# Kernel optimization log

Hardware: AMD Instinct MI355X
Metric: run time of the kernel (lower is better)

The kernel has to match this reference:

```python
import jax, jax.numpy as jnp
import numpy as np

B, C, H, W = 8, 256, 128, 128
SH, SW = 8, 8            # stoken_size
HH, WW = H // SH, W // SW
NH = 8                   # num_heads
HD = C // NH             # head_dim = 32
KD = HD                  # key_dim (attn_ratio=1)
ATTN_SCALE = KD ** (-0.5)
AFF_SCALE = C ** (-0.5)


def unfold9(x):
    """x: (B,C,hh,ww) -> (B, hh*ww, C, 9); matches Unfold(3) + transpose/reshape."""
    b, c, hh, ww = x.shape
    xp = jnp.pad(x, ((0, 0), (0, 0), (1, 1), (1, 1)))
    p = jnp.stack([xp[:, :, dy:dy + hh, dx:dx + ww]
                   for dy in range(3) for dx in range(3)], axis=2)  # (B,C,9,hh,ww)
    return p.transpose(0, 3, 4, 1, 2).reshape(b, hh * ww, c, 9)


def fold9(y):
    """y: (B,C,9,hh,ww) -> (B,C,hh,ww); matches Fold(3) (conv_transpose with identity kernels)."""
    hh, ww = y.shape[-2:]
    yp = jnp.pad(y, ((0, 0), (0, 0), (0, 0), (1, 1), (1, 1)))
    out = 0.
    for dy in range(3):
        for dx in range(3):
            out = out + yp[:, :, dy * 3 + dx, 2 - dy:2 - dy + hh, 2 - dx:2 - dx + ww]
    return out


def attention(sf, w_qkv, w_pe, w_proj):
    """Attention module with attn_ratio=1 (Conv layers have act=False, BN identity)."""
    b, c, hh, ww = sf.shape
    n = hh * ww
    qkv = jnp.einsum('oc,bchw->bohw', w_qkv, sf).reshape(b, NH, 2 * KD + HD, n)
    q, k, v = jnp.split(qkv, [KD, 2 * KD], axis=2)
    attn = jax.nn.softmax(jnp.einsum('bhkn,bhkm->bhnm', q, k) * ATTN_SCALE, axis=-1)
    o = jnp.einsum('bhdm,bhnm->bhdn', v, attn).reshape(b, c, hh, ww)
    pe = jax.lax.conv_general_dilated(
        v.reshape(b, c, hh, ww), w_pe, (1, 1), ((1, 1), (1, 1)),
        dimension_numbers=('NCHW', 'OIHW', 'NCHW'), feature_group_count=c)
    return jnp.einsum('oc,bchw->bohw', w_proj, o + pe)


def setup_inputs() -> dict:
    key = jax.random.key(0)
    k0, k1, k2, k3 = jax.random.split(key, 4)
    x = jax.random.normal(k0, (B, C, H, W), dtype=jnp.float32)
    w_qkv = jax.random.normal(k1, (3 * C, C), dtype=jnp.float32) * 0.05
    w_pe = jax.random.normal(k2, (C, 1, 3, 3), dtype=jnp.float32) * 0.05
    w_proj = jax.random.normal(k3, (C, C), dtype=jnp.float32) * 0.05
    return {'x': x, 'w_qkv': w_qkv, 'w_pe': w_pe, 'w_proj': w_proj}


def reference(x, w_qkv, w_pe, w_proj):
    # H,W divisible by stoken_size -> no padding branch
    xb = x.reshape(B, C, HH, SH, WW, SW)
    stoken = xb.mean(axis=(3, 5))                                   # (B,C,hh,ww) adaptive_avg_pool2d
    pix = xb.transpose(0, 2, 4, 3, 5, 1).reshape(B, HH * WW, SH * SW, C)
    # --- single no-grad iteration (n_iter=1) ---
    sf9 = unfold9(stoken)                                            # (B,n,C,9)
    aff = jax.nn.softmax(jnp.einsum('bnpc,bnck->bnpk', pix, sf9) * AFF_SCALE, axis=-1)
    aff = jax.lax.stop_gradient(aff)                                 # torch.no_grad
    asum = aff.sum(axis=2).transpose(0, 2, 1).reshape(B, 1, 9, HH, WW)
    asum = jax.lax.stop_gradient(fold9(asum))                        # (B,1,hh,ww)
    # --- super-token aggregation ---
    sf = jnp.einsum('bnpc,bnpk->bnck', pix, aff)                     # (B,n,C,9)
    sf = fold9(sf.transpose(0, 2, 3, 1).reshape(B, C, 9, HH, WW))    # (B,C,hh,ww)
    sf = sf / (asum + 1e-12)
    # --- refine with attention ---
    sf = attention(sf, w_qkv, w_pe, w_proj)
    # --- scatter back to pixels ---
    sf9b = unfold9(sf)                                               # (B,n,C,9)
    pix_out = jnp.einsum('bnck,bnpk->bnpc', sf9b, aff)               # (B,n,h*w,C)
    return pix_out.reshape(B, HH, WW, C, SH, SW).transpose(0, 3, 1, 4, 2, 5).reshape(B, C, H, W)
```

## Files before the change

kernel.cpp:

```cpp
#include <hip/hip_runtime.h>
#include <cstdint>
#include <cstddef>


#define AFF_SCALE 0.0625f
#define ATTN_SCALE 0.17677669529663687f

__global__ __launch_bounds__(128) void stoken_kernel(
    const float* __restrict__ x, float* __restrict__ stok_pad)
{
    int blk = blockIdx.x;
    int i  = blk & 15;
    int bc = blk >> 4;
    int t  = threadIdx.x;
    const float* xr = x + ((size_t)bc * 128 + i * 8) * 128 + t;
    float s = 0.f;
#pragma unroll
    for (int r = 0; r < 8; ++r) s += xr[r * 128];
    s += __shfl_down(s, 4, 64);
    s += __shfl_down(s, 2, 64);
    s += __shfl_down(s, 1, 64);
    if ((t & 7) == 0) {
        int j = t >> 3;
        stok_pad[((size_t)bc * 18 + (i + 1)) * 18 + (j + 1)] = s * (1.f / 64.f);
    }
}

__global__ __launch_bounds__(256) void aff_agg_kernel(
    const float* __restrict__ x, const float* __restrict__ stok_pad,
    float* __restrict__ aff_g, float* __restrict__ asum_g,
    float* __restrict__ agg)
{
    __shared__ float pixs[256 * 65];
    __shared__ float part[4 * 64 * 9];
    __shared__ float affs[9 * 64];

    int bn = blockIdx.x;
    int n = bn & 255, b = bn >> 8;
    int i = n >> 4, j = n & 15;
    int t = threadIdx.x;

    {
        int c0 = t >> 3, pi = t & 7;
#pragma unroll
        for (int it = 0; it < 8; ++it) {
            int c = c0 + 32 * it;
            const float* xp = x + (((size_t)b * 256 + c) * 128 + i * 8 + pi) * 128 + j * 8;
            const float4 f0 = *(const float4*)&xp[0];
            const float4 f1 = *(const float4*)&xp[4];
            float* d = &pixs[c * 65 + pi * 8];
            d[0] = f0.x; d[1] = f0.y; d[2] = f0.z; d[3] = f0.w;
            d[4] = f1.x; d[5] = f1.y; d[6] = f1.z; d[7] = f1.w;
        }
    }
    __syncthreads();

    int s = t >> 6, p = t & 63;
    float acc[9] = {0.f,0.f,0.f,0.f,0.f,0.f,0.f,0.f,0.f};
    {
        const float* sp = stok_pad + ((size_t)b * 256 + s * 64) * 324 + i * 18 + j;
        for (int cc = 0; cc < 64; ++cc) {
            float px = pixs[(s * 64 + cc) * 65 + p];
            const float* q = sp + cc * 324;
            acc[0] += px * q[0];  acc[1] += px * q[1];  acc[2] += px * q[2];
            acc[3] += px * q[18]; acc[4] += px * q[19]; acc[5] += px * q[20];
            acc[6] += px * q[36]; acc[7] += px * q[37]; acc[8] += px * q[38];
        }
    }
#pragma unroll
    for (int k = 0; k < 9; ++k) part[(s * 64 + p) * 9 + k] = acc[k];
    __syncthreads();

    if (t < 64) {
        float a[9];
        float mx = -1e30f;
#pragma unroll
        for (int k = 0; k < 9; ++k) {
            float v = (part[(0 * 64 + t) * 9 + k] + part[(1 * 64 + t) * 9 + k] +
                       part[(2 * 64 + t) * 9 + k] + part[(3 * 64 + t) * 9 + k]) * AFF_SCALE;
            a[k] = v;
            mx = fmaxf(mx, v);
        }
        float ssum = 0.f;
#pragma unroll
        for (int k = 0; k < 9; ++k) { a[k] = __expf(a[k] - mx); ssum += a[k]; }
        float inv = 1.f / ssum;
#pragma unroll
        for (int k = 0; k < 9; ++k) {
            a[k] *= inv;
            affs[k * 64 + t] = a[k];
            aff_g[(size_t)bn * 576 + k * 64 + t] = a[k];
        }
#pragma unroll
        for (int k = 0; k < 9; ++k) {
            float r = a[k];
            r += __shfl_down(r, 32, 64); r += __shfl_down(r, 16, 64);
            r += __shfl_down(r, 8, 64);  r += __shfl_down(r, 4, 64);
            r += __shfl_down(r, 2, 64);  r += __shfl_down(r, 1, 64);
            if (t == 0) asum_g[(size_t)bn * 9 + k] = r;
        }
    }
    __syncthreads();

    {
        int c = t;
        float a9[9] = {0.f,0.f,0.f,0.f,0.f,0.f,0.f,0.f,0.f};
        for (int p4 = 0; p4 < 16; ++p4) {
            float px0 = pixs[c * 65 + p4 * 4 + 0];
            float px1 = pixs[c * 65 + p4 * 4 + 1];
            float px2 = pixs[c * 65 + p4 * 4 + 2];
            float px3 = pixs[c * 65 + p4 * 4 + 3];
#pragma unroll
            for (int k = 0; k < 9; ++k) {
                const float4 av = *(const float4*)&affs[k * 64 + p4 * 4];
                a9[k] += px0 * av.x + px1 * av.y + px2 * av.z + px3 * av.w;
            }
        }
#pragma unroll
        for (int k = 0; k < 9; ++k)
            agg[((size_t)bn * 9 + k) * 256 + c] = a9[k];
    }
}

__global__ __launch_bounds__(256) void fold_div_kernel(
    const float* __restrict__ agg, const float* __restrict__ asum_g,
    float* __restrict__ sf)
{
    __shared__ float v[256 * 17];
    int b = blockIdx.x >> 4, y = blockIdx.x & 15;
    int t = threadIdx.x;
    for (int x = 0; x < 16; ++x) {
        float af = 0.f, val = 0.f;
#pragma unroll
        for (int dy = 0; dy < 3; ++dy)
#pragma unroll
            for (int dx = 0; dx < 3; ++dx) {
                int ii = y + 1 - dy, jj = x + 1 - dx;
                if ((unsigned)ii < 16u && (unsigned)jj < 16u) {
                    int idx = (b * 256 + ii * 16 + jj) * 9 + dy * 3 + dx;
                    af  += asum_g[idx];
                    val += agg[(size_t)idx * 256 + t];
                }
            }
        v[t * 17 + x] = val / (af + 1e-12f);
    }
    __syncthreads();
    int xw = t & 15, cw0 = t >> 4;
#pragma unroll
    for (int it = 0; it < 16; ++it) {
        int c = cw0 + it * 16;
        sf[((size_t)b * 256 + c) * 256 + y * 16 + xw] = v[c * 17 + xw];
    }
}

__global__ __launch_bounds__(256) void gemm_w(
    const float* __restrict__ A, const float* __restrict__ Bm,
    float* __restrict__ Cout, int M, int mode)
{
    __shared__ float As[32 * 68];
    __shared__ float Bs[32 * 64];
    int b = blockIdx.x, o0 = blockIdx.y * 64, n0 = blockIdx.z * 64;
    int t = threadIdx.x;
    int tr = t >> 4, tc = t & 15;
    const float* Bb = Bm + (size_t)b * 256 * 256;
    float acc[4][4];
#pragma unroll
    for (int ii = 0; ii < 4; ++ii)
#pragma unroll
        for (int jj = 0; jj < 4; ++jj) acc[ii][jj] = 0.f;

    for (int k0 = 0; k0 < 256; k0 += 32) {
        {
            int ol = t >> 2, kq = (t & 3) * 8;
            const float* Ap = A + (size_t)(o0 + ol) * 256 + k0 + kq;
            const float4 f0 = *(const float4*)&Ap[0];
            const float4 f1 = *(const float4*)&Ap[4];
            As[(kq + 0) * 68 + ol] = f0.x; As[(kq + 1) * 68 + ol] = f0.y;
            As[(kq + 2) * 68 + ol] = f0.z; As[(kq + 3) * 68 + ol] = f0.w;
            As[(kq + 4) * 68 + ol] = f1.x; As[(kq + 5) * 68 + ol] = f1.y;
            As[(kq + 6) * 68 + ol] = f1.z; As[(kq + 7) * 68 + ol] = f1.w;
        }
#pragma unroll
        for (int i2 = 0; i2 < 8; ++i2) {
            int e = t + i2 * 256;
            int kl = e >> 6, nl = e & 63;
            Bs[kl * 64 + nl] = Bb[(size_t)(k0 + kl) * 256 + n0 + nl];
        }
        __syncthreads();
#pragma unroll
        for (int kk = 0; kk < 32; ++kk) {
            const float4 av = *(const float4*)&As[kk * 68 + tr * 4];
            const float4 bv = *(const float4*)&Bs[kk * 64 + tc * 4];
            acc[0][0] += av.x * bv.x; acc[0][1] += av.x * bv.y; acc[0][2] += av.x * bv.z; acc[0][3] += av.x * bv.w;
            acc[1][0] += av.y * bv.x; acc[1][1] += av.y * bv.y; acc[1][2] += av.y * bv.z; acc[1][3] += av.y * bv.w;
            acc[2][0] += av.z * bv.x; acc[2][1] += av.z * bv.y; acc[2][2] += av.z * bv.z; acc[2][3] += av.z * bv.w;
            acc[3][0] += av.w * bv.x; acc[3][1] += av.w * bv.y; acc[3][2] += av.w * bv.z; acc[3][3] += av.w * bv.w;
        }
        __syncthreads();
    }

    if (mode == 0) {
#pragma unroll
        for (int ii = 0; ii < 4; ++ii) {
            int o = o0 + tr * 4 + ii;
            float4 st = make_float4(acc[ii][0], acc[ii][1], acc[ii][2], acc[ii][3]);
            *(float4*)&Cout[((size_t)b * M + o) * 256 + n0 + tc * 4] = st;
        }
    } else {
#pragma unroll
        for (int jj = 0; jj < 4; ++jj) {
            int n = n0 + tc * 4 + jj;
            int y = n >> 4, x = n & 15;
            float4 st = make_float4(acc[0][jj], acc[1][jj], acc[2][jj], acc[3][jj]);
            *(float4*)&Cout[(((size_t)b * 18 + 1 + y) * 18 + 1 + x) * 256 + o0 + tr * 4] = st;
        }
    }
}

__global__ __launch_bounds__(256) void attn_kernel(
    const float* __restrict__ qkv, float* __restrict__ o_attn)
{
    __shared__ float smem[9216];
    int b = blockIdx.x, h = blockIdx.y, nt = blockIdx.z;
    int t = threadIdx.x, nl = t & 63, mq = t >> 6;
    int n = nt * 64 + nl;

    {
        int dd = t >> 3, mb = (t & 7) * 32;
        const float* krow = qkv + ((size_t)b * 768 + h * 96 + 32 + dd) * 256;
#pragma unroll
        for (int e4 = 0; e4 < 8; ++e4) {
            int m = mb + e4 * 4;
            const float4 kw = *(const float4*)&krow[m];
            smem[(m + 0) * 32 + dd] = kw.x; smem[(m + 1) * 32 + dd] = kw.y;
            smem[(m + 2) * 32 + dd] = kw.z; smem[(m + 3) * 32 + dd] = kw.w;
        }
    }
    float q[32];
    {
        const float* qbase = qkv + ((size_t)b * 768 + h * 96) * 256 + n;
#pragma unroll
        for (int d = 0; d < 32; ++d) q[d] = qbase[(size_t)d * 256];
    }
    __syncthreads();

    float l[64];
#pragma unroll
    for (int e = 0; e < 64; ++e) {
        const float* kp = &smem[(mq * 64 + e) * 32];
        float s = 0.f;
#pragma unroll
        for (int d4 = 0; d4 < 8; ++d4) {
            const float4 kv4 = *(const float4*)&kp[d4 * 4];
            s += q[d4 * 4 + 0] * kv4.x + q[d4 * 4 + 1] * kv4.y +
                 q[d4 * 4 + 2] * kv4.z + q[d4 * 4 + 3] * kv4.w;
        }
        l[e] = s * ATTN_SCALE;
    }
    float mx = -1e30f;
#pragma unroll
    for (int e = 0; e < 64; ++e) mx = fmaxf(mx, l[e]);
    float sm = 0.f;
#pragma unroll
    for (int e = 0; e < 64; ++e) { l[e] = __expf(l[e] - mx); sm += l[e]; }
    __syncthreads();

    {
        int dd = t >> 3, mb = (t & 7) * 32;
        const float* vrow = qkv + ((size_t)b * 768 + h * 96 + 64 + dd) * 256;
#pragma unroll
        for (int e4 = 0; e4 < 8; ++e4) {
            int m = mb + e4 * 4;
            const float4 vw = *(const float4*)&vrow[m];
            smem[(m + 0) * 32 + dd] = vw.x; smem[(m + 1) * 32 + dd] = vw.y;
            smem[(m + 2) * 32 + dd] = vw.z; smem[(m + 3) * 32 + dd] = vw.w;
        }
    }
    __syncthreads();

    float oa[32];
#pragma unroll
    for (int d = 0; d < 32; ++d) oa[d] = 0.f;
#pragma unroll
    for (int e = 0; e < 64; ++e) {
        float pm = l[e];
        const float* vp = &smem[(mq * 64 + e) * 32];
#pragma unroll
        for (int d4 = 0; d4 < 8; ++d4) {
            const float4 vv = *(const float4*)&vp[d4 * 4];
            oa[d4 * 4 + 0] += pm * vv.x; oa[d4 * 4 + 1] += pm * vv.y;
            oa[d4 * 4 + 2] += pm * vv.z; oa[d4 * 4 + 3] += pm * vv.w;
        }
    }
    __syncthreads();

    float* op   = smem;
    float* mxsm = smem + 8448;
    {
        int idx = mq * 64 + nl;
#pragma unroll
        for (int d = 0; d < 32; ++d) op[idx * 33 + d] = oa[d];
        mxsm[idx * 2 + 0] = mx;
        mxsm[idx * 2 + 1] = sm;
    }
    __syncthreads();

    if (t < 64) {
        float M2 = -1e30f;
#pragma unroll
        for (int q4 = 0; q4 < 4; ++q4) M2 = fmaxf(M2, mxsm[(q4 * 64 + t) * 2]);
        float w[4], S = 0.f;
#pragma unroll
        for (int q4 = 0; q4 < 4; ++q4) {
            w[q4] = __expf(mxsm[(q4 * 64 + t) * 2] - M2);
            S += mxsm[(q4 * 64 + t) * 2 + 1] * w[q4];
        }
        float inv = 1.f / S;
#pragma unroll
        for (int d = 0; d < 32; ++d) {
            float o = 0.f;
#pragma unroll
            for (int q4 = 0; q4 < 4; ++q4) o += op[(q4 * 64 + t) * 33 + d] * w[q4];
            o_attn[((size_t)b * 256 + h * 32 + d) * 256 + nt * 64 + t] = o * inv;
        }
    }
}

__global__ __launch_bounds__(256) void peadd_kernel(
    const float* __restrict__ qkv, const float* __restrict__ w_pe,
    float* __restrict__ o_attn)
{
    int bc = blockIdx.x;
    int b = bc >> 8, c = bc & 255;
    int t = threadIdx.x;
    int y = t >> 4, x = t & 15;
    int h = c >> 5, d = c & 31;
    const float* v = qkv + ((size_t)b * 768 + h * 96 + 64 + d) * 256;
    float acc = o_attn[(size_t)bc * 256 + t];
#pragma unroll
    for (int ky = 0; ky < 3; ++ky)
#pragma unroll
        for (int kx = 0; kx < 3; ++kx) {
            int yy = y + ky - 1, xx = x + kx - 1;
            if ((unsigned)yy < 16u && (unsigned)xx < 16u)
                acc += w_pe[c * 9 + ky * 3 + kx] * v[yy * 16 + xx];
        }
    o_attn[(size_t)bc * 256 + t] = acc;
}

__global__ __launch_bounds__(256) void scatter_kernel(
    const float* __restrict__ sfa_pad, const float* __restrict__ aff_g,
    float* __restrict__ out)
{
    __shared__ float ss[3 * 18 * 40];
    __shared__ float aff_s[16 * 577];

    int blk = blockIdx.x;
    int pi = blk & 7, i = (blk >> 3) & 15, b = blk >> 7;
    int t = threadIdx.x;

    for (int e = t; e < 1728; e += 256) {
        int dy = e / 576, rem = e % 576;
        int col = rem >> 5, idx = rem & 31;
        int q = idx >> 3, d = idx & 7;
        ss[(dy * 18 + col) * 40 + idx] =
            sfa_pad[(((size_t)b * 18 + i + dy) * 18 + col) * 256 + q * 64 + pi * 8 + d];
    }
    {
        const float* ag = aff_g + ((size_t)b * 256 + i * 16) * 576;
        for (int e = t; e < 9216; e += 256) {
            int j = e / 576, rem = e % 576;
            int k = rem >> 6, p = rem & 63;
            aff_s[j * 577 + p * 9 + k] = ag[j * 576 + rem];
        }
    }
    __syncthreads();

    int lane = t & 63, w = t >> 6;
    int j0 = lane >> 3, pj = lane & 7;
    int j1 = j0 + 8;

    float S0[4][9], S1[4][9];
#pragma unroll
    for (int q = 0; q < 4; ++q)
#pragma unroll
        for (int k = 0; k < 9; ++k) {
            int dy = k / 3, dx = k % 3;
            S0[q][k] = ss[(dy * 18 + j0 + dx) * 40 + q * 8 + pj];
            S1[q][k] = ss[(dy * 18 + j1 + dx) * 40 + q * 8 + pj];
        }

    int y = i * 8 + pi;
    size_t ob = (size_t)b * 256 * 16384 + (size_t)y * 128;
    const float* A0 = &aff_s[j0 * 577];
    const float* A1 = &aff_s[j1 * 577];
    for (int p = w * 16; p < w * 16 + 16; ++p) {
        float a0[9], a1[9];
#pragma unroll
        for (int k = 0; k < 9; ++k) { a0[k] = A0[p * 9 + k]; a1[k] = A1[p * 9 + k]; }
#pragma unroll
        for (int q = 0; q < 4; ++q) {
            int c2 = p * 4 + q;
            float v0 = 0.f, v1 = 0.f;
#pragma unroll
            for (int k = 0; k < 9; ++k) {
                v0 += S0[q][k] * a0[k];
                v1 += S1[q][k] * a1[k];
            }
            out[ob + (size_t)c2 * 16384 + lane] = v0;
            out[ob + (size_t)c2 * 16384 + 64 + lane] = v1;
        }
    }
}

extern "C" void kernel_launch(void* const* d_in, const int* in_sizes, int n_in,
                              void* d_out, int out_size, void* d_ws, size_t ws_size,
                              hipStream_t stream) {
    const float* x      = (const float*)d_in[0];
    const float* w_qkv  = (const float*)d_in[1];
    const float* w_pe   = (const float*)d_in[2];
    const float* w_proj = (const float*)d_in[3];
    float* out = (float*)d_out;
    float* agg = (float*)d_out;

    float* ws = (float*)d_ws;
    const size_t o_aff  = 0;
    const size_t o_asum = 1179648;
    const size_t o_pad  = 1198080;
    const size_t o_sf   = 1861632;
    const size_t o_qkv  = 2385920;

    hipMemsetAsync(ws + o_pad, 0, 663552 * sizeof(float), stream);

    stoken_kernel<<<8 * 256 * 16, 128, 0, stream>>>(x, ws + o_pad);
    aff_agg_kernel<<<8 * 256, 256, 0, stream>>>(x, ws + o_pad, ws + o_aff,
                                                ws + o_asum, agg);
    fold_div_kernel<<<8 * 16, 256, 0, stream>>>(agg, ws + o_asum, ws + o_sf);
    gemm_w<<<dim3(8, 12, 4), 256, 0, stream>>>(w_qkv, ws + o_sf, ws + o_qkv, 768, 0);
    hipMemsetAsync(ws + o_pad, 0, 663552 * sizeof(float), stream);
    attn_kernel<<<dim3(8, 8, 4), 256, 0, stream>>>(ws + o_qkv, ws + o_sf);
    peadd_kernel<<<8 * 256, 256, 0, stream>>>(ws + o_qkv, w_pe, ws + o_sf);
    gemm_w<<<dim3(8, 4, 4), 256, 0, stream>>>(w_proj, ws + o_sf, ws + o_pad, 256, 1);
    scatter_kernel<<<8 * 16 * 8, 256, 0, stream>>>(ws + o_pad, ws + o_aff, out);
}
```

Baseline: 495.4 us.

## Restructure affinity kernel: stage super-tokens in LDS, pad rows, swizzle blocks per XCD

The affinity/aggregation kernel now stages the 9 neighbouring super-token vectors in shared memory instead of reading them from global memory inside the inner loop. The pixel tile uses a 68-float row pitch so loads and stores can be float4-vectorised, and the aggregation loop is rotated per channel group to spread LDS bank accesses. Partial sums are combined with shared-memory atomics rather than a 4-way reduction buffer. Block indices are remapped so that neighbouring super-tokens land on the same XCD, which should improve L2 reuse of the input rows. The costs are LDS atomic contention and a larger shared-memory footprint, which may reduce occupancy.

```diff
diff --git a/kernel.cpp b/kernel.cpp
--- a/kernel.cpp
+++ b/kernel.cpp
@@ -31,13 +31,16 @@
     float* __restrict__ aff_g, float* __restrict__ asum_g,
     float* __restrict__ agg)
 {
-    __shared__ float pixs[256 * 65];
-    __shared__ float part[4 * 64 * 9];
-    __shared__ float affs[9 * 64];
-
-    int bn = blockIdx.x;
-    int n = bn & 255, b = bn >> 8;
-    int i = n >> 4, j = n & 15;
+    __shared__ __align__(16) float pixs[256 * 68];
+    __shared__ __align__(16) float sfs[9 * 260];
+    __shared__ __align__(16) float part[64 * 9];
+
+    int bid  = blockIdx.x;
+    int xcd  = bid & 7, slot = bid >> 3;
+    int pair = xcd * 128 + (slot >> 1);
+    int m = pair & 7, i = (pair >> 3) & 15, b = pair >> 7;
+    int j = m * 2 + (slot & 1);
+    int bn = b * 256 + i * 16 + j;
     int t = threadIdx.x;
 
     {
@@ -46,38 +49,54 @@
         for (int it = 0; it < 8; ++it) {
             int c = c0 + 32 * it;
             const float* xp = x + (((size_t)b * 256 + c) * 128 + i * 8 + pi) * 128 + j * 8;
-            const float4 f0 = *(const float4*)&xp[0];
-            const float4 f1 = *(const float4*)&xp[4];
-            float* d = &pixs[c * 65 + pi * 8];
-            d[0] = f0.x; d[1] = f0.y; d[2] = f0.z; d[3] = f0.w;
-            d[4] = f1.x; d[5] = f1.y; d[6] = f1.z; d[7] = f1.w;
-        }
-    }
-    __syncthreads();
-
-    int s = t >> 6, p = t & 63;
-    float acc[9] = {0.f,0.f,0.f,0.f,0.f,0.f,0.f,0.f,0.f};
-    {
-        const float* sp = stok_pad + ((size_t)b * 256 + s * 64) * 324 + i * 18 + j;
-        for (int cc = 0; cc < 64; ++cc) {
-            float px = pixs[(s * 64 + cc) * 65 + p];
-            const float* q = sp + cc * 324;
-            acc[0] += px * q[0];  acc[1] += px * q[1];  acc[2] += px * q[2];
-            acc[3] += px * q[18]; acc[4] += px * q[19]; acc[5] += px * q[20];
-            acc[6] += px * q[36]; acc[7] += px * q[37]; acc[8] += px * q[38];
-        }
-    }
-#pragma unroll
-    for (int k = 0; k < 9; ++k) part[(s * 64 + p) * 9 + k] = acc[k];
-    __syncthreads();
+            float4 f0 = *(const float4*)&xp[0];
+            float4 f1 = *(const float4*)&xp[4];
+            *(float4*)&pixs[c * 68 + pi * 8]     = f0;
+            *(float4*)&pixs[c * 68 + pi * 8 + 4] = f1;
+        }
+    }
+    {
+        const float* sp = stok_pad + ((size_t)b * 256 + t) * 324 + i * 18 + j;
+#pragma unroll
+        for (int dy = 0; dy < 3; ++dy)
+#pragma unroll
+            for (int dx = 0; dx < 3; ++dx)
+                sfs[(dy * 3 + dx) * 260 + t] = sp[dy * 18 + dx];
+    }
+    part[t] = 0.f;
+    part[t + 256] = 0.f;
+    if (t < 64) part[t + 512] = 0.f;
+    __syncthreads();
+
+    {
+        int s = t >> 6, p = t & 63;
+        float acc[9] = {0.f,0.f,0.f,0.f,0.f,0.f,0.f,0.f,0.f};
+        int cb = s * 64;
+        for (int c4 = 0; c4 < 64; c4 += 4) {
+            int c = cb + c4;
+            float px0 = pixs[(c + 0) * 68 + p];
+            float px1 = pixs[(c + 1) * 68 + p];
+            float px2 = pixs[(c + 2) * 68 + p];
+            float px3 = pixs[(c + 3) * 68 + p];
+#pragma unroll
+            for (int k = 0; k < 9; ++k) {
+                const float4 sv = *(const float4*)&sfs[k * 260 + c];
+                acc[k] += px0 * sv.x + px1 * sv.y + px2 * sv.z + px3 * sv.w;
+            }
+        }
+#pragma unroll
+        for (int k = 0; k < 9; ++k) atomicAdd(&part[p * 9 + k], acc[k]);
+    }
+    __syncthreads();
+
+    float* affs = sfs;
 
     if (t < 64) {
         float a[9];
         float mx = -1e30f;
 #pragma unroll
         for (int k = 0; k < 9; ++k) {
-            float v = (part[(0 * 64 + t) * 9 + k] + part[(1 * 64 + t) * 9 + k] +
-                       part[(2 * 64 + t) * 9 + k] + part[(3 * 64 + t) * 9 + k]) * AFF_SCALE;
+            float v = part[t * 9 + k] * AFF_SCALE;
             a[k] = v;
             mx = fmaxf(mx, v);
         }
@@ -104,16 +123,15 @@
 
     {
         int c = t;
+        int rot = (c >> 3) & 15;
         float a9[9] = {0.f,0.f,0.f,0.f,0.f,0.f,0.f,0.f,0.f};
-        for (int p4 = 0; p4 < 16; ++p4) {
-            float px0 = pixs[c * 65 + p4 * 4 + 0];
-            float px1 = pixs[c * 65 + p4 * 4 + 1];
-            float px2 = pixs[c * 65 + p4 * 4 + 2];
-            float px3 = pixs[c * 65 + p4 * 4 + 3];
+        for (int p4i = 0; p4i < 16; ++p4i) {
+            int p4 = (p4i + rot) & 15;
+            const float4 pv = *(const float4*)&pixs[c * 68 + p4 * 4];
 #pragma unroll
             for (int k = 0; k < 9; ++k) {
                 const float4 av = *(const float4*)&affs[k * 64 + p4 * 4];
-                a9[k] += px0 * av.x + px1 * av.y + px2 * av.z + px3 * av.w;
+                a9[k] += pv.x * av.x + pv.y * av.y + pv.z * av.z + pv.w * av.w;
             }
         }
 #pragma unroll
```

Result: faster. 447.3 us (-9.7%).
